# Kernel tuning notes

Hardware: AMD Instinct MI355X
Metric: run time of the kernel (lower is better)

## Reference

```python
import jax, jax.numpy as jnp
import numpy as np

B, N, CIN = 16, 2048, 6
R, G = 20, 128          # Reeb nodes, scc group size
F1 = 1000
NCLASS = 40


def pairwise_distance(pc):
    # pc: (B, N, C) -> adjacency exp(-squared_euclidean_dist), (B, N, N)
    inner = -2.0 * jnp.matmul(pc, pc.transpose(0, 2, 1))
    sq = jnp.sum(pc * pc, axis=-1, keepdims=True)
    return jnp.exp(-(sq + inner + sq.transpose(0, 2, 1)))


def get_laplacian(adj):
    # normalized Laplacian L = I - D^{-1/2} A D^{-1/2}
    d_inv = 1.0 / jnp.sqrt(jnp.sum(adj, axis=-1))
    eye = jnp.eye(adj.shape[-1], dtype=adj.dtype)
    return eye - d_inv[:, :, None] * adj * d_inv[:, None, :]


def cheb_conv(x, L, K, W, b):
    # Chebyshev recurrence: T0=x, T1=Lx, Tk=2L T_{k-1} - T_{k-2}
    xs = [x]
    if K > 1:
        x0, x1 = x, jnp.matmul(L, x)
        xs.append(x1)
        for _ in range(2, K):
            x2 = 2.0 * jnp.matmul(L, x1) - x0
            xs.append(x2)
            x0, x1 = x1, x2
    Bb, Nn, Fin = x.shape
    # torch stacks on dim0 then permutes to (B,N,Fin,K) before reshape -> K is minor axis
    xk = jnp.stack(xs, axis=-1).reshape(Bb, Nn, Fin * K)
    return jnp.matmul(xk, W) + b


def setup_inputs() -> dict:
    key = jax.random.key(0)
    ks = jax.random.split(key, 10)

    def glorot(k, shape):
        lim = np.sqrt(6.0 / (shape[0] + shape[1])).astype(np.float32)
        return jax.random.uniform(k, shape, jnp.float32, -lim, lim)

    return {
        "x": jax.random.normal(ks[0], (B, N, CIN), jnp.float32),
        "laplacian_Reeb": jax.random.normal(ks[1], (B, R, R), jnp.float32),
        "sccs": jax.random.randint(ks[2], (B, R, G), 0, N),
        "W1": glorot(ks[3], (CIN * 3, F1)), "b1": jnp.zeros((F1,), jnp.float32),
        "W2": glorot(ks[4], (F1 * 3, F1)), "b2": jnp.zeros((F1,), jnp.float32),
        "Wr": glorot(ks[5], (F1 * 6, F1)), "br": jnp.zeros((F1,), jnp.float32),
        "Wfc1": glorot(ks[6], (2 * F1, 512)), "bfc1": jnp.zeros((512,), jnp.float32),
        "Wfc2": glorot(ks[7], (512, 128)), "bfc2": jnp.zeros((128,), jnp.float32),
        "Wfc3": glorot(ks[8], (128, NCLASS)), "bfc3": jnp.zeros((NCLASS,), jnp.float32),
        "k": 30, "batch_size": B, "num_points": N,
    }


def reference(x, laplacian_Reeb, sccs, W1, b1, W2, b2, Wr, br,
              Wfc1, bfc1, Wfc2, bfc2, Wfc3, bfc3, k, batch_size, num_points):
    regs = []
    # graph Laplacian from point features (torch.no_grad)
    L = jax.lax.stop_gradient(get_laplacian(pairwise_distance(x)))
    out = jax.nn.relu(cheb_conv(x, L, 3, W1, b1))
    regs.append(jnp.linalg.norm(jnp.matmul(jnp.matmul(out.transpose(0, 2, 1), L), x)))

    # Reeb pooling: per Reeb node, max over its scc vertex group (torch.no_grad)
    v = out[jnp.arange(out.shape[0])[:, None, None], sccs]  # (B, R, G, F1)
    vertices_Reeb = jax.lax.stop_gradient(jnp.max(v, axis=2))  # (B, R, F1)

    # second dynamic-graph Laplacian on features (torch.no_grad)
    L2 = jax.lax.stop_gradient(get_laplacian(pairwise_distance(out)))
    out2 = jax.nn.relu(cheb_conv(out, L2, 3, W2, b2))
    regs.append(jnp.linalg.norm(jnp.matmul(jnp.matmul(out2.transpose(0, 2, 1), L2), x)))

    out_Reeb = jax.nn.relu(cheb_conv(vertices_Reeb, laplacian_Reeb, 6, Wr, br))

    g = jnp.max(out2, axis=1)           # (B, F1) global max pool
    g_Reeb = jnp.max(out_Reeb, axis=1)  # (B, F1)
    feat = jnp.concatenate([g_Reeb, g], axis=1)  # (B, 2000)

    h = jax.nn.relu(jnp.matmul(feat, Wfc1) + bfc1)
    regs += [jnp.sum(Wfc1[:, 0] ** 2), bfc1[0] ** 2]  # norm(weight.data[0])**2
    h = jax.nn.relu(jnp.matmul(h, Wfc2) + bfc2)
    regs += [jnp.sum(Wfc2[:, 0] ** 2), bfc2[0] ** 2]
    out_final = jnp.matmul(h, Wfc3) + bfc3
    regs += [jnp.sum(Wfc3[:, 0] ** 2), bfc3[0] ** 2]

    return out_final, jnp.stack(regs)
```

## Files before the change

### kernel.cpp

```cpp
#include <hip/hip_runtime.h>
#include <stdint.h>

#define DI __device__ __forceinline__

typedef __bf16 bf16x8 __attribute__((ext_vector_type(8)));
typedef float f32x4 __attribute__((ext_vector_type(4)));
typedef unsigned short u16x4 __attribute__((ext_vector_type(4)));
typedef unsigned short u16x8 __attribute__((ext_vector_type(8)));

static constexpr int BB = 16;
static constexpr int NP = 2048;
static constexpr int FP = 1024;
static constexpr int K3 = 3072;
static constexpr int RR = 20;
static constexpr int GG = 128;
static constexpr int RK = 6144;
static constexpr int MRp = 384;
static constexpr int NJ = 32;
static constexpr int NI = 8;
static constexpr int NJ2 = 8;
static constexpr int TPAD = 132;

DI float b2f(unsigned short u) {
    unsigned v = ((unsigned)u) << 16;
    return __builtin_bit_cast(float, v);
}
DI unsigned short f2b(float f) {
    unsigned u = __builtin_bit_cast(unsigned, f);
    unsigned r = (u + 0x7FFFu + ((u >> 16) & 1u)) >> 16;
    return (unsigned short)r;
}

DI void glds16(const unsigned short* g, unsigned short* l) {
    __builtin_amdgcn_global_load_lds(
        (const __attribute__((address_space(1))) void*)g,
        (__attribute__((address_space(3))) void*)l, 16, 0, 0);
}

#define SYNC_VM4() asm volatile("s_waitcnt vmcnt(4)\n\ts_barrier" ::: "memory")
#define SYNC_VM0() asm volatile("s_waitcnt vmcnt(0)\n\ts_barrier" ::: "memory")
#define SYNC_LGKM() asm volatile("s_waitcnt lgkmcnt(0)\n\ts_barrier" ::: "memory")

enum { EADJ = 0, ELAP1 = 1, ELAP2 = 2, EBRELU = 3, EACCR = 4 };

template <int EPI>
__global__ __launch_bounds__(256) void gemm_bt(
    const unsigned short* __restrict__ A, long sA, int lda,
    const unsigned short* __restrict__ Bt, long sB, int ldb,
    unsigned short* __restrict__ C, long sC, int ldc, int K,
    const float* __restrict__ sq,
    float* __restrict__ rowsum,
    const unsigned short* __restrict__ aux, long sAux, int ldaux,
    const float* __restrict__ bias, int biasN)
{
    __shared__ unsigned short smem[128 * TPAD];
    const int tid = threadIdx.x;

    int gx = gridDim.x, gy = gridDim.y;
    int flat = blockIdx.x + gx * (blockIdx.y + gy * blockIdx.z);
    int tpb = gx * gy;
    int T = tpb * gridDim.z;
    int bz, ty, tx;
    if (((T & 7) == 0) && ((gx & 7) == 0)) {
        int per = T >> 3;
        int g = (flat & 7) * per + (flat >> 3);
        bz = g / tpb;
        int t = g - bz * tpb;
        int strip = gy << 3;
        int cg = t / strip;
        int r = t - cg * strip;
        ty = r >> 3;
        tx = (cg << 3) + (r & 7);
    } else {
        bz = blockIdx.z; ty = blockIdx.y; tx = blockIdx.x;
    }
    bool diag = true;
    if (EPI == EADJ) {
        int t = tx;
        int qx = 0;
        while ((qx + 1) * (qx + 2) / 2 <= t) qx++;
        ty = t - qx * (qx + 1) / 2;
        tx = qx;
        diag = (ty == tx);
    }
    const int rowBase = ty * 128;
    const int colBase = tx * 128;
    const unsigned short* Ab;
    const unsigned short* Bb;
    if (EPI == EACCR) {
        Ab = A + (long)rowBase * lda + (long)bz * K;
        Bb = Bt + (long)colBase * ldb + (long)bz * K;
    } else {
        Ab = A + (long)bz * sA + (long)rowBase * lda;
        Bb = Bt + (long)bz * sB + (long)colBase * ldb;
    }

    const int lane = tid & 63;
    const int q = lane >> 4;
    const int l15 = lane & 15;
    const int wave = tid >> 6;
    const int wr = (wave >> 1) * 64;
    const int wc = (wave & 1) * 64;

    const int r0 = tid & 127, c0 = tid >> 7;
    const int c1 = c0 + 2;

    f32x4 acc[4][4];
#pragma unroll
    for (int i = 0; i < 4; i++)
#pragma unroll
        for (int j = 0; j < 4; j++) acc[i][j] = f32x4{0.f, 0.f, 0.f, 0.f};

    const int nIter = K >> 5;
    glds16(Ab + (long)r0 * lda + c0 * 8, smem + tid * 8);
    glds16(Ab + (long)r0 * lda + c1 * 8, smem + (tid + 256) * 8);
    glds16(Bb + (long)r0 * ldb + c0 * 8, smem + 4096 + tid * 8);
    glds16(Bb + (long)r0 * ldb + c1 * 8, smem + 4096 + (tid + 256) * 8);

    for (int it = 0; it < nIter; ++it) {
        unsigned short* cur = smem + ((it & 1) << 13);
        unsigned short* nxt = smem + (((it + 1) & 1) << 13);
        if (it + 1 < nIter) {
            const int kb = (it + 1) << 5;
            glds16(Ab + (long)r0 * lda + kb + c0 * 8, nxt + tid * 8);
            glds16(Ab + (long)r0 * lda + kb + c1 * 8, nxt + (tid + 256) * 8);
            glds16(Bb + (long)r0 * ldb + kb + c0 * 8, nxt + 4096 + tid * 8);
            glds16(Bb + (long)r0 * ldb + kb + c1 * 8, nxt + 4096 + (tid + 256) * 8);
            SYNC_VM4();
        } else {
            SYNC_VM0();
        }
        bf16x8 af[4], bfr[4];
#pragma unroll
        for (int mi = 0; mi < 4; mi++)
            af[mi] = *(const bf16x8*)(cur + (q * 128 + wr + mi * 16 + l15) * 8);
#pragma unroll
        for (int ni = 0; ni < 4; ni++)
            bfr[ni] = *(const bf16x8*)(cur + 4096 + (q * 128 + wc + ni * 16 + l15) * 8);
#pragma unroll
        for (int mi = 0; mi < 4; mi++)
#pragma unroll
            for (int ni = 0; ni < 4; ni++)
                acc[mi][ni] = __builtin_amdgcn_mfma_f32_16x16x32_bf16(
                    af[mi], bfr[ni], acc[mi][ni], 0, 0, 0);
        SYNC_LGKM();
    }

    if (EPI == EADJ) __syncthreads();

    const float* sqb = (EPI == EADJ || EPI == ELAP1 || EPI == ELAP2)
                           ? (sq + (long)bz * NP) : nullptr;
#pragma unroll
    for (int mi = 0; mi < 4; mi++) {
#pragma unroll
        for (int rg = 0; rg < 4; rg++) {
            const int grow = rowBase + wr + mi * 16 + q * 4 + rg;
            float rsumv = 0.f;
            float di = 0.f;
            if (EPI == ELAP1 || EPI == ELAP2) di = sqb[grow];
#pragma unroll
            for (int ni = 0; ni < 4; ni++) {
                const int gcol = colBase + wc + ni * 16 + l15;
                float v = acc[mi][ni][rg];
                long cidx = (long)bz * sC + (long)grow * ldc + gcol;
                if (EPI == EADJ) {
                    float e = __expf(2.f * v - sqb[grow] - sqb[gcol]);
                    unsigned short h = f2b(e);
                    C[cidx] = h;
                    rsumv += e;
                    if (!diag) {
                        const int rl = wr + mi * 16 + q * 4 + rg;
                        const int cl = wc + ni * 16 + l15;
                        smem[cl * TPAD + rl] = h;
                    }
                } else if (EPI == ELAP1) {
                    float o = b2f(aux[(long)bz * sAux + (long)grow * ldaux + gcol]);
                    C[cidx] = f2b(o - di * v);
                } else if (EPI == ELAP2) {
                    long abase = (long)bz * sAux + (long)grow * ldaux + gcol;
                    float o0 = b2f(aux[abase]);
                    float o1 = b2f(aux[abase + 1024]);
                    C[cidx] = f2b(2.f * (o1 - di * v) - o0);
                } else if (EPI == EBRELU) {
                    float bv = (gcol < biasN) ? bias[gcol] : 0.f;
                    float o = v + bv;
                    C[cidx] = f2b(o > 0.f ? o : 0.f);
                } else {
                    atomicAdd(&rowsum[(long)grow * ldc + gcol], v);
                }
            }
            if (EPI == EADJ) {
                rsumv += __shfl_xor(rsumv, 1);
                rsumv += __shfl_xor(rsumv, 2);
                rsumv += __shfl_xor(rsumv, 4);
                rsumv += __shfl_xor(rsumv, 8);
                if (l15 == 0) atomicAdd(&rowsum[(long)bz * NP + grow], rsumv);
            }
        }
    }

    if (EPI == EADJ) {
        if (!diag) {
            __syncthreads();
            const int cl = tid >> 1, hh = tid & 1;
            const unsigned short* srcp = smem + cl * TPAD + hh * 64;
            unsigned short* dstp = C + (long)bz * sC + (long)(colBase + cl) * ldc
                                 + rowBase + hh * 64;
            float csum = 0.f;
#pragma unroll
            for (int k2 = 0; k2 < 8; k2++) {
                u16x4 v0 = *(const u16x4*)(srcp + k2 * 8);
                u16x4 v1 = *(const u16x4*)(srcp + k2 * 8 + 4);
                u16x8 vv;
                vv[0] = v0[0]; vv[1] = v0[1]; vv[2] = v0[2]; vv[3] = v0[3];
                vv[4] = v1[0]; vv[5] = v1[1]; vv[6] = v1[2]; vv[7] = v1[3];
#pragma unroll
                for (int e2 = 0; e2 < 8; e2++) csum += b2f(vv[e2]);
                *(u16x8*)(dstp + k2 * 8) = vv;
            }
            atomicAdd(&rowsum[(long)bz * NP + colBase + cl], csum);
        }
    }
}

__global__ __launch_bounds__(256) void k_trs(
    const unsigned short* __restrict__ src, long sS, int ldS,
    const float* __restrict__ dv,
    unsigned short* __restrict__ dst, long sD, int ldD)
{
    __shared__ unsigned short t[64][72];
    const int b = blockIdx.z;
    const int c0 = blockIdx.x * 64, r0 = blockIdx.y * 64;
    const unsigned short* S = src + (long)b * sS;
    const float* dvb = dv + (long)b * NP;
    unsigned short* D = dst + (long)b * sD;
    const int tx = threadIdx.x & 7, ty = threadIdx.x >> 3;
#pragma unroll
    for (int p = 0; p < 2; p++) {
        int r = ty + p * 32;
        float s = dvb[r0 + r];
        u16x8 v = *(const u16x8*)(S + (long)(r0 + r) * ldS + c0 + tx * 8);
#pragma unroll
        for (int k = 0; k < 8; k++) t[tx * 8 + k][r] = f2b(s * b2f(v[k]));
    }
    __syncthreads();
#pragma unroll
    for (int p = 0; p < 2; p++) {
        int r = ty + p * 32;
        u16x8 v;
#pragma unroll
        for (int k = 0; k < 8; k++) v[k] = t[r][tx * 8 + k];
        *(u16x8*)(D + (long)(c0 + r) * ldD + r0 + tx * 8) = v;
    }
}

__global__ void k_trf32(const float* __restrict__ src, int R, int C,
                        float* __restrict__ dst)
{
    __shared__ float t[32][33];
    const int c0 = blockIdx.x * 32, r0 = blockIdx.y * 32;
#pragma unroll
    for (int p = 0; p < 4; p++) {
        int r = r0 + threadIdx.y + p * 8;
        int c = c0 + threadIdx.x;
        t[threadIdx.y + p * 8][threadIdx.x] =
            (r < R && c < C) ? src[(long)r * C + c] : 0.f;
    }
    __syncthreads();
#pragma unroll
    for (int p = 0; p < 4; p++) {
        int c = c0 + threadIdx.y + p * 8;
        int r = r0 + threadIdx.x;
        if (c < C && r < R) dst[(long)c * R + r] = t[threadIdx.x][threadIdx.y + p * 8];
    }
}

__global__ __launch_bounds__(256) void k_wperm(
    const float* __restrict__ W, unsigned short* __restrict__ dst, int KK, int dstld)
{
    __shared__ float tile[64][65];
    const int o0 = blockIdx.x * 64;
    const int kk0 = blockIdx.y * 64;
    const int s = kk0 >> 10;
    const int fbase = kk0 & 1023;
    const int ci = threadIdx.x & 63;
    const int ri = threadIdx.x >> 6;
#pragma unroll 4
    for (int p = 0; p < 16; p++) {
        int fi = fbase + ri + p * 4;
        int oi = o0 + ci;
        float v = 0.f;
        if (fi < 1000 && oi < 1000) v = W[((long)fi * KK + s) * 1000 + oi];
        tile[ri + p * 4][ci] = v;
    }
    __syncthreads();
#pragma unroll 4
    for (int p = 0; p < 16; p++) {
        int orow = ri + p * 4;
        dst[(long)(o0 + orow) * dstld + kk0 + ci] = f2b(tile[ci][orow]);
    }
}

__global__ void k_zinit(float* __restrict__ rs2, float* __restrict__ g,
                        float* __restrict__ racc, unsigned short* __restrict__ catrpad,
                        float* __restrict__ dv1, float* __restrict__ xacc1,
                        float* __restrict__ xacc2, float* __restrict__ yacc1,
                        float* __restrict__ yacc2, float* __restrict__ l2acc,
                        float* __restrict__ vr, float* __restrict__ sqc,
                        float* __restrict__ accR)
{
    long i = (long)blockIdx.x * 256 + threadIdx.x;
    if (i < (long)BB * NP) { rs2[i] = 0.f; dv1[i] = 0.f; sqc[i] = 0.f; }
    if (i < (long)BB * FP) g[i] = 0.f;
    if (i < 64) racc[i] = 0.f;
    if (i < (long)(MRp - 320) * RK) catrpad[i] = 0;
    if (i < (long)BB * 6 * NP) { xacc1[i] = 0.f; xacc2[i] = 0.f; l2acc[i] = 0.f; }
    if (i < (long)BB * 6 * FP) { yacc1[i] = 0.f; yacc2[i] = 0.f; }
    if (i < (long)BB * RR * FP) vr[i] = 0.f;
    if (i < (long)MRp * FP) accR[i] = 0.f;
}

__global__ void k_xprep(const float* __restrict__ x, float* __restrict__ x6t,
                        float* __restrict__ sqx)
{
    const int b = blockIdx.y;
    const int j = blockIdx.x * 256 + threadIdx.x;
    float s = 0.f;
#pragma unroll
    for (int c = 0; c < 6; c++) {
        float v = x[((long)b * NP + j) * 6 + c];
        x6t[(long)b * 6 * NP + c * NP + j] = v;
        s += v * v;
    }
    sqx[(long)b * NP + j] = s;
}

template <int MODE>
__global__ __launch_bounds__(256) void k_lapj(
    const float* __restrict__ x6t, const float* __restrict__ sqx,
    const float* __restrict__ dv1, const float* __restrict__ srct,
    float* __restrict__ acc)
{
    const int b = blockIdx.z;
    const int row = blockIdx.x * 256 + threadIdx.x;
    const int j0 = blockIdx.y * (NP / NJ);
    const float* xt = x6t + (long)b * 6 * NP;
    const float* sq = sqx + (long)b * NP;
    float xi[6];
#pragma unroll
    for (int c = 0; c < 6; c++) xi[c] = xt[c * NP + row];
    const float sqi = sq[row];
    const float* dv = (MODE >= 1) ? (dv1 + (long)b * NP) : nullptr;
    const float* st = (MODE >= 1) ? (srct + (long)b * 6 * NP) : nullptr;
    float s0 = 0.f;
    float sc[6] = {0, 0, 0, 0, 0, 0};
    for (int j = j0; j < j0 + NP / NJ; j++) {
        float dot = 0.f;
#pragma unroll
        for (int c = 0; c < 6; c++) dot += xi[c] * xt[c * NP + j];
        float e = __expf(2.f * dot - sqi - sq[j]);
        if (MODE == 0) {
            s0 += e;
        } else {
            float wgt = e * dv[j];
#pragma unroll
            for (int c = 0; c < 6; c++) sc[c] += wgt * st[c * NP + j];
        }
    }
    if (MODE == 0) {
        atomicAdd(&acc[(long)b * NP + row], s0);
    } else {
#pragma unroll
        for (int c = 0; c < 6; c++)
            atomicAdd(&acc[(long)b * 6 * NP + c * NP + row], sc[c]);
    }
}

template <int MODE>
__global__ void k_lfin(const float* __restrict__ x6t, const float* __restrict__ dv1,
                       const float* __restrict__ xacc, const float* __restrict__ x1t6,
                       float* __restrict__ outv)
{
    const int b = blockIdx.y;
    const int row = blockIdx.x * 256 + threadIdx.x;
    const float di = dv1[(long)b * NP + row];
#pragma unroll
    for (int c = 0; c < 6; c++) {
        long idx = (long)b * 6 * NP + c * NP + row;
        float xi = x6t[idx];
        float sc = xacc[idx];
        if (MODE == 1) outv[idx] = xi - di * sc;
        else           outv[idx] = 2.f * (x1t6[idx] - di * sc) - xi;
    }
}

__global__ __launch_bounds__(256) void k_adjx(
    const unsigned short* __restrict__ adj, const float* __restrict__ dv,
    const float* __restrict__ x6t, float* __restrict__ l2acc)
{
    __shared__ float xs[6][256];
    __shared__ float dvs[256];
    __shared__ float lsum[64][4][6];
    const int b = blockIdx.z;
    const int j0 = blockIdx.y * (NP / NJ2);
    if (threadIdx.x < 256) dvs[threadIdx.x] = dv[(long)b * NP + j0 + threadIdx.x];
    for (int e = threadIdx.x; e < 6 * 256; e += 256) {
        int c = e >> 8, j = e & 255;
        xs[c][j] = x6t[(long)b * 6 * NP + c * NP + j0 + j];
    }
    __syncthreads();
    const int ty = threadIdx.x >> 2;
    const int tx = threadIdx.x & 3;
    const int grow = blockIdx.x * 64 + ty;
    const unsigned short* rowp = adj + (long)b * NP * NP + (long)grow * NP + j0;
    float sc[6] = {0, 0, 0, 0, 0, 0};
    for (int it = 0; it < 8; it++) {
        int col = it * 32 + tx * 8;
        u16x8 a8 = *(const u16x8*)(rowp + col);
#pragma unroll
        for (int k = 0; k < 8; k++) {
            float w = b2f(a8[k]) * dvs[col + k];
#pragma unroll
            for (int c = 0; c < 6; c++) sc[c] += w * xs[c][col + k];
        }
    }
#pragma unroll
    for (int c = 0; c < 6; c++) lsum[ty][tx][c] = sc[c];
    __syncthreads();
    for (int e = threadIdx.x; e < 64 * 6; e += 256) {
        int row = e / 6, c = e % 6;
        float t = lsum[row][0][c] + lsum[row][1][c] + lsum[row][2][c] + lsum[row][3][c];
        atomicAdd(&l2acc[(long)b * 6 * NP + (long)c * NP + blockIdx.x * 64 + row], t);
    }
}

__global__ __launch_bounds__(256) void k_cheb1(
    const float* __restrict__ x, const float* __restrict__ x1t6,
    const float* __restrict__ x2t6, const float* __restrict__ W1,
    const float* __restrict__ b1, unsigned short* __restrict__ cat,
    float* __restrict__ sqc)
{
    __shared__ float xk[128 * 18];
    __shared__ float rs[128];
    const int b = blockIdx.z;
    const int n0 = blockIdx.x * 128;
    const int f0 = blockIdx.y * 256;
    for (int e = threadIdx.x; e < 128 * 18; e += 256) {
        int rown = e / 18, c18 = e % 18;
        int cc = c18 / 3, kk = c18 % 3;
        int n = n0 + rown;
        float v;
        if (kk == 0) v = x[((long)b * NP + n) * 6 + cc];
        else if (kk == 1) v = x1t6[(long)b * 6 * NP + cc * NP + n];
        else v = x2t6[(long)b * 6 * NP + cc * NP + n];
        xk[e] = v;
    }
    if (threadIdx.x < 128) rs[threadIdx.x] = 0.f;
    __syncthreads();
    const int lane = threadIdx.x & 63;
    for (int gi = threadIdx.x; gi < 128 * 64; gi += 256) {
        int rown = gi >> 6;
        int f4 = f0 + (gi & 63) * 4;
        float a0 = 0, a1 = 0, a2 = 0, a3 = 0;
        if (f4 < 1000) {
            a0 = b1[f4]; a1 = b1[f4 + 1]; a2 = b1[f4 + 2]; a3 = b1[f4 + 3];
#pragma unroll
            for (int cI = 0; cI < 18; cI++) {
                float xv = xk[rown * 18 + cI];
                f32x4 w = *(const f32x4*)(W1 + cI * 1000 + f4);
                a0 += xv * w[0]; a1 += xv * w[1]; a2 += xv * w[2]; a3 += xv * w[3];
            }
            a0 = a0 > 0 ? a0 : 0; a1 = a1 > 0 ? a1 : 0;
            a2 = a2 > 0 ? a2 : 0; a3 = a3 > 0 ? a3 : 0;
        }
        u16x4 o;
        o[0] = f2b(a0); o[1] = f2b(a1); o[2] = f2b(a2); o[3] = f2b(a3);
        *(u16x4*)(cat + (long)b * NP * K3 + (long)(n0 + rown) * K3 + f4) = o;
        float r0 = b2f(o[0]), r1 = b2f(o[1]), r2 = b2f(o[2]), r3 = b2f(o[3]);
        float s2 = r0 * r0 + r1 * r1 + r2 * r2 + r3 * r3;
#pragma unroll
        for (int d = 1; d < 64; d <<= 1) s2 += __shfl_xor(s2, d);
        if (lane == 0) atomicAdd(&rs[rown], s2);
    }
    __syncthreads();
    if (threadIdx.x < 128)
        atomicAdd(&sqc[(long)b * NP + n0 + threadIdx.x], rs[threadIdx.x]);
}

__global__ void k_rsqrt(float* __restrict__ p) {
    int i = blockIdx.x * 256 + threadIdx.x;
    p[i] = rsqrtf(p[i]);
}

__global__ void k_vr(const unsigned short* __restrict__ cat,
                     const int* __restrict__ sccs, float* __restrict__ vr)
{
    const int b = blockIdx.y, r = blockIdx.x;
    const int g0 = blockIdx.z * (GG / 4);
    const int f4 = threadIdx.x * 4;
    const int* sp = sccs + ((long)b * RR + r) * GG;
    float m0 = 0.f, m1 = 0.f, m2 = 0.f, m3 = 0.f;
    for (int g = g0; g < g0 + GG / 4; g++) {
        int idx = sp[g];
        u16x4 v = *(const u16x4*)(cat + ((long)b * NP + idx) * K3 + f4);
        m0 = fmaxf(m0, b2f(v[0])); m1 = fmaxf(m1, b2f(v[1]));
        m2 = fmaxf(m2, b2f(v[2])); m3 = fmaxf(m3, b2f(v[3]));
    }
    float* op = vr + ((long)b * RR + r) * FP + f4;
    atomicMax((int*)&op[0], __float_as_int(m0));
    atomicMax((int*)&op[1], __float_as_int(m1));
    atomicMax((int*)&op[2], __float_as_int(m2));
    atomicMax((int*)&op[3], __float_as_int(m3));
}

__global__ __launch_bounds__(256) void k_reeb(
    const float* __restrict__ vr, const float* __restrict__ lapR,
    unsigned short* __restrict__ catr)
{
    __shared__ float Lr[RR * RR];
    const int b = blockIdx.y;
    for (int e = threadIdx.x; e < RR * RR; e += 256) Lr[e] = lapR[(long)b * RR * RR + e];
    __syncthreads();
    const int f = blockIdx.x * 256 + threadIdx.x;
    float xa[RR], xb[RR], xc[RR];
#pragma unroll
    for (int r = 0; r < RR; r++) xa[r] = vr[((long)b * RR + r) * FP + f];
#pragma unroll
    for (int r = 0; r < RR; r++) catr[((long)b * RR + r) * RK + f] = f2b(xa[r]);
#pragma unroll
    for (int r = 0; r < RR; r++) {
        float s = 0.f;
#pragma unroll
        for (int qq = 0; qq < RR; qq++) s += Lr[r * RR + qq] * xa[qq];
        xb[r] = s;
    }
#pragma unroll
    for (int r = 0; r < RR; r++) catr[((long)b * RR + r) * RK + FP + f] = f2b(xb[r]);
    for (int st = 2; st < 6; st++) {
#pragma unroll
        for (int r = 0; r < RR; r++) {
            float s = 0.f;
#pragma unroll
            for (int qq = 0; qq < RR; qq++) s += Lr[r * RR + qq] * xb[qq];
            xc[r] = 2.f * s - xa[r];
        }
#pragma unroll
        for (int r = 0; r < RR; r++)
            catr[((long)b * RR + r) * RK + st * FP + f] = f2b(xc[r]);
#pragma unroll
        for (int r = 0; r < RR; r++) { xa[r] = xb[r]; xb[r] = xc[r]; }
    }
}

__global__ void k_rfin(const float* __restrict__ accR, const float* __restrict__ br,
                       unsigned short* __restrict__ outr)
{
    const int f = blockIdx.x * 256 + threadIdx.x;
    const int m = blockIdx.y;
    float bv = (f < 1000) ? br[f] : 0.f;
    float v = accR[(long)m * FP + f] + bv;
    outr[(long)m * FP + f] = f2b(v > 0.f ? v : 0.f);
}

__global__ void k_grmax(const unsigned short* __restrict__ outr, float* __restrict__ gr)
{
    const int b = blockIdx.y;
    const int f = blockIdx.x * 256 + threadIdx.x;
    float m = -1e30f;
    for (int r = 0; r < RR; r++)
        m = fmaxf(m, b2f(outr[((long)b * RR + r) * FP + f]));
    gr[(long)b * FP + f] = (f < 1000) ? m : 0.f;
}

__global__ __launch_bounds__(256) void k_rnacc(
    const unsigned short* __restrict__ mat, long sM, int ldm,
    const float* __restrict__ vt6, float* __restrict__ yacc,
    float* __restrict__ gm)
{
    const int b = blockIdx.z;
    const int f = blockIdx.x * 256 + threadIdx.x;
    const int i0 = blockIdx.y * (NP / NI);
    const unsigned short* mp = mat + (long)b * sM + f;
    const float* vp = vt6 + (long)b * 6 * NP;
    float a[6] = {0, 0, 0, 0, 0, 0};
    float mx = 0.f;
    for (int i = i0; i < i0 + NP / NI; i++) {
        float o = b2f(mp[(long)i * ldm]);
        if (gm) mx = fmaxf(mx, o);
#pragma unroll
        for (int c = 0; c < 6; c++) a[c] += o * vp[c * NP + i];
    }
#pragma unroll
    for (int c = 0; c < 6; c++)
        atomicAdd(&yacc[((long)b * 6 + c) * FP + f], a[c]);
    if (gm) atomicMax((int*)&gm[(long)b * FP + f], __float_as_int(mx));
}

__global__ void k_rnred(const float* __restrict__ yacc1,
                        const float* __restrict__ yacc2, float* __restrict__ racc)
{
    __shared__ float red[256];
    const float* y = (blockIdx.x == 0) ? yacc1 : yacc2;
    const long tot = (long)BB * 6 * FP;
    const long per = tot / 16;
    const long e0 = blockIdx.y * per;
    float s = 0.f;
    for (long e = e0 + threadIdx.x; e < e0 + per; e += 256) {
        float v = y[e];
        s += v * v;
    }
    red[threadIdx.x] = s;
    __syncthreads();
    for (int st = 128; st > 0; st >>= 1) {
        if (threadIdx.x < st) red[threadIdx.x] += red[threadIdx.x + st];
        __syncthreads();
    }
    if (threadIdx.x == 0) atomicAdd(&racc[blockIdx.x], red[0]);
}

__global__ __launch_bounds__(256) void k_fc1w(
    const float* __restrict__ gr, const float* __restrict__ g,
    const float* __restrict__ WT1, const float* __restrict__ bias,
    float* __restrict__ h1)
{
    const int b = blockIdx.y;
    const int lane = threadIdx.x & 63;
    const int o = blockIdx.x * 4 + (threadIdx.x >> 6);
    const float* wt = WT1 + (long)o * 2000;
    const float* grp = gr + (long)b * FP;
    const float* gp = g + (long)b * FP;
    float s = 0.f;
    for (int j0 = 0; j0 < 2000; j0 += 64) {
        int j = j0 + lane;
        if (j < 2000) {
            float fv = (j < 1000) ? grp[j] : gp[j - 1000];
            s += fv * wt[j];
        }
    }
#pragma unroll
    for (int d = 1; d < 64; d <<= 1) s += __shfl_xor(s, d);
    if (lane == 0) {
        float v = s + bias[o];
        h1[(long)b * 512 + o] = v > 0.f ? v : 0.f;
    }
}

__global__ __launch_bounds__(256) void k_fc2w(
    const float* __restrict__ h1, const float* __restrict__ WT2,
    const float* __restrict__ bias, float* __restrict__ h2)
{
    const int b = blockIdx.y;
    const int lane = threadIdx.x & 63;
    const int o = blockIdx.x * 4 + (threadIdx.x >> 6);
    const float* wt = WT2 + (long)o * 512;
    const float* hp = h1 + (long)b * 512;
    float s = 0.f;
#pragma unroll
    for (int j0 = 0; j0 < 512; j0 += 64) s += hp[j0 + lane] * wt[j0 + lane];
#pragma unroll
    for (int d = 1; d < 64; d <<= 1) s += __shfl_xor(s, d);
    if (lane == 0) {
        float v = s + bias[o];
        h2[(long)b * 128 + o] = v > 0.f ? v : 0.f;
    }
}

__global__ void k_tail(const float* __restrict__ h2, const float* __restrict__ Wfc3,
                       const float* __restrict__ bfc3, const float* __restrict__ Wfc1,
                       const float* __restrict__ bfc1, const float* __restrict__ Wfc2,
                       const float* __restrict__ bfc2, const float* __restrict__ racc,
                       float* __restrict__ out)
{
    if (blockIdx.x == 0) {
        for (int e = threadIdx.x; e < 640; e += 256) {
            int row = e / 40, o = e % 40;
            float s = bfc3[o];
            for (int j = 0; j < 128; j++) s += h2[row * 128 + j] * Wfc3[j * 40 + o];
            out[e] = s;
        }
        return;
    }
    __shared__ float red[256];
    float s = 0.f;
    if (blockIdx.x == 1) {
        for (int j = threadIdx.x; j < 2000; j += 256) { float w = Wfc1[j * 512]; s += w * w; }
    } else if (blockIdx.x == 2) {
        for (int j = threadIdx.x; j < 512; j += 256) { float w = Wfc2[j * 128]; s += w * w; }
    } else {
        for (int j = threadIdx.x; j < 128; j += 256) { float w = Wfc3[j * 40]; s += w * w; }
    }
    red[threadIdx.x] = s;
    __syncthreads();
    for (int st = 128; st > 0; st >>= 1) {
        if (threadIdx.x < st) red[threadIdx.x] += red[threadIdx.x + st];
        __syncthreads();
    }
    if (threadIdx.x == 0) {
        if (blockIdx.x == 1) out[642] = red[0];
        else if (blockIdx.x == 2) out[644] = red[0];
        else {
            out[646] = red[0];
            out[640] = sqrtf(racc[0]);
            out[641] = sqrtf(racc[1]);
            out[643] = bfc1[0] * bfc1[0];
            out[645] = bfc2[0] * bfc2[0];
            out[647] = bfc3[0] * bfc3[0];
        }
    }
}

extern "C" void kernel_launch(void* const* d_in, const int* in_sizes, int n_in,
                              void* d_out, int out_size, void* d_ws, size_t ws_size,
                              hipStream_t stream)
{
    (void)in_sizes; (void)n_in; (void)out_size;
    const float* x    = (const float*)d_in[0];
    const float* lapR = (const float*)d_in[1];
    const int*   sccs = (const int*)d_in[2];
    const float* W1   = (const float*)d_in[3];
    const float* b1   = (const float*)d_in[4];
    const float* W2   = (const float*)d_in[5];
    const float* b2   = (const float*)d_in[6];
    const float* Wr   = (const float*)d_in[7];
    const float* br   = (const float*)d_in[8];
    const float* Wfc1 = (const float*)d_in[9];
    const float* bfc1 = (const float*)d_in[10];
    const float* Wfc2 = (const float*)d_in[11];
    const float* bfc2 = (const float*)d_in[12];
    const float* Wfc3 = (const float*)d_in[13];
    const float* bfc3 = (const float*)d_in[14];
    float* out = (float*)d_out;

    char* w = (char*)d_ws;
    size_t used = 0;
    auto alloc = [&](size_t bytes) {
        char* p = w + used;
        used += (bytes + 255) & ~(size_t)255;
        return p;
    };
    unsigned short* w2pt = (unsigned short*)alloc((size_t)FP * K3 * 2);
    unsigned short* wrpt = (unsigned short*)alloc((size_t)FP * RK * 2);
    unsigned short* catr = (unsigned short*)alloc((size_t)MRp * RK * 2);
    unsigned short* outr = (unsigned short*)alloc((size_t)MRp * FP * 2);
    float* accR = (float*)alloc((size_t)MRp * FP * 4);
    float* vr   = (float*)alloc((size_t)BB * RR * FP * 4);
    float* x6t  = (float*)alloc((size_t)BB * 6 * NP * 4);
    float* sqx  = (float*)alloc((size_t)BB * NP * 4);
    float* dv1  = (float*)alloc((size_t)BB * NP * 4);
    float* x1t6 = (float*)alloc((size_t)BB * 6 * NP * 4);
    float* x2t6 = (float*)alloc((size_t)BB * 6 * NP * 4);
    float* xacc1= (float*)alloc((size_t)BB * 6 * NP * 4);
    float* xacc2= (float*)alloc((size_t)BB * 6 * NP * 4);
    float* l2acc= (float*)alloc((size_t)BB * 6 * NP * 4);
    float* sqc  = (float*)alloc((size_t)BB * NP * 4);
    float* rs2  = (float*)alloc((size_t)BB * NP * 4);
    float* l2xt6= (float*)alloc((size_t)BB * 6 * NP * 4);
    float* g    = (float*)alloc((size_t)BB * FP * 4);
    float* gr   = (float*)alloc((size_t)BB * FP * 4);
    float* h1   = (float*)alloc((size_t)BB * 512 * 4);
    float* h2   = (float*)alloc((size_t)BB * 128 * 4);
    float* racc = (float*)alloc(256);
    float* WT1  = (float*)alloc((size_t)512 * 2000 * 4);
    float* WT2  = (float*)alloc((size_t)128 * 512 * 4);
    float* yacc1= (float*)alloc((size_t)BB * 6 * FP * 4);
    float* yacc2= (float*)alloc((size_t)BB * 6 * FP * 4);

    const size_t PCAT = (size_t)NP * K3 * 2;
    const size_t PA   = (size_t)NP * NP * 2;
    const size_t PTT  = (size_t)FP * NP * 2;
    int C = 16;
    while (C > 1 && used + (size_t)C * (PCAT + PA + PTT) + 4096 > ws_size) C >>= 1;
    if (used + (size_t)C * (PCAT + PA + PTT) + 4096 > ws_size) return;

    unsigned short* cat_c = (unsigned short*)alloc((size_t)C * PCAT);
    unsigned short* a_c   = (unsigned short*)alloc((size_t)C * PA);
    unsigned short* tt_c  = (unsigned short*)alloc((size_t)C * PTT);
    unsigned short* out2_c = a_c;

    const long sCat = (long)NP * K3;
    const long sL2  = (long)NP * NP;
    const long sTT  = (long)FP * NP;
    const long sO2  = (long)NP * FP;

    k_zinit<<<dim3(1536), 256, 0, stream>>>(rs2, g, racc, catr + (size_t)320 * RK,
                                            dv1, xacc1, xacc2, yacc1, yacc2, l2acc,
                                            vr, sqc, accR);

    k_wperm<<<dim3(16, K3 / 64), 256, 0, stream>>>(W2, w2pt, 3, K3);
    k_wperm<<<dim3(16, RK / 64), 256, 0, stream>>>(Wr, wrpt, 6, RK);
    k_trf32<<<dim3(16, 63), dim3(32, 8), 0, stream>>>(Wfc1, 2000, 512, WT1);
    k_trf32<<<dim3(4, 16), dim3(32, 8), 0, stream>>>(Wfc2, 512, 128, WT2);

    k_xprep<<<dim3(8, BB), 256, 0, stream>>>(x, x6t, sqx);
    k_lapj<0><<<dim3(8, NJ, BB), 256, 0, stream>>>(x6t, sqx, nullptr, nullptr, dv1);
    k_rsqrt<<<dim3(BB * NP / 256), 256, 0, stream>>>(dv1);
    k_lapj<1><<<dim3(8, NJ, BB), 256, 0, stream>>>(x6t, sqx, dv1, x6t, xacc1);
    k_lfin<1><<<dim3(8, BB), 256, 0, stream>>>(x6t, dv1, xacc1, nullptr, x1t6);
    k_lapj<2><<<dim3(8, NJ, BB), 256, 0, stream>>>(x6t, sqx, dv1, x1t6, xacc2);
    k_lfin<2><<<dim3(8, BB), 256, 0, stream>>>(x6t, dv1, xacc2, x1t6, x2t6);

    for (int c0 = 0; c0 < BB; c0 += C) {
        const float* xc  = x     + (long)c0 * NP * 6;
        const float* x6c = x6t   + (long)c0 * 6 * NP;
        const float* x1c = x1t6  + (long)c0 * 6 * NP;
        const float* x2c = x2t6  + (long)c0 * 6 * NP;
        float*       sqcc= sqc   + (long)c0 * NP;
        float*       rsc = rs2   + (long)c0 * NP;
        float*       l2ac= l2acc + (long)c0 * 6 * NP;
        float*       l2xc= l2xt6 + (long)c0 * 6 * NP;

        k_cheb1<<<dim3(16, 4, C), 256, 0, stream>>>(xc, x1c, x2c, W1, b1, cat_c, sqcc);

        gemm_bt<EADJ><<<dim3(136, 1, C), 256, 0, stream>>>(
            cat_c, sCat, K3, cat_c, sCat, K3, a_c, sL2, NP, FP,
            sqcc, rsc, nullptr, 0, 0, nullptr, 0);
        k_rsqrt<<<dim3(C * NP / 256), 256, 0, stream>>>(rsc);

        k_adjx<<<dim3(NP / 64, NJ2, C), 256, 0, stream>>>(a_c, rsc, x6c, l2ac);
        k_lfin<1><<<dim3(8, C), 256, 0, stream>>>(x6c, rsc, l2ac, nullptr, l2xc);

        k_trs<<<dim3(16, 32, C), 256, 0, stream>>>(cat_c, sCat, K3, rsc, tt_c, sTT, NP);
        gemm_bt<ELAP1><<<dim3(8, 16, C), 256, 0, stream>>>(
            a_c, sL2, NP, tt_c, sTT, NP, cat_c + 1024, sCat, K3, NP,
            rsc, nullptr, cat_c, sCat, K3, nullptr, 0);

        k_trs<<<dim3(16, 32, C), 256, 0, stream>>>(cat_c + 1024, sCat, K3, rsc, tt_c, sTT, NP);
        gemm_bt<ELAP2><<<dim3(8, 16, C), 256, 0, stream>>>(
            a_c, sL2, NP, tt_c, sTT, NP, cat_c + 2048, sCat, K3, NP,
            rsc, nullptr, cat_c, sCat, K3, nullptr, 0);

        gemm_bt<EBRELU><<<dim3(8, 16, C), 256, 0, stream>>>(
            cat_c, sCat, K3, w2pt, 0, K3, out2_c, sO2, FP, K3,
            nullptr, nullptr, nullptr, 0, 0, b2, 1000);

        k_vr<<<dim3(RR, C, 4), 256, 0, stream>>>(
            cat_c, sccs + (long)c0 * RR * GG, vr + (long)c0 * RR * FP);
        k_rnacc<<<dim3(4, NI, C), 256, 0, stream>>>(
            cat_c, sCat, K3, x1c, yacc1 + (long)c0 * 6 * FP, nullptr);
        k_rnacc<<<dim3(4, NI, C), 256, 0, stream>>>(
            out2_c, sO2, FP, l2xc, yacc2 + (long)c0 * 6 * FP, g + (long)c0 * FP);
    }

    k_reeb<<<dim3(4, BB), 256, 0, stream>>>(vr, lapR, catr);
    gemm_bt<EACCR><<<dim3(8, 3, 4), 256, 0, stream>>>(
        catr, 0, RK, wrpt, 0, RK, outr, 0, FP, RK / 4,
        nullptr, accR, nullptr, 0, 0, nullptr, 0);
    k_rfin<<<dim3(4, 320), 256, 0, stream>>>(accR, br, outr);
    k_grmax<<<dim3(4, BB), 256, 0, stream>>>(outr, gr);

    k_rnred<<<dim3(2, 16), 256, 0, stream>>>(yacc1, yacc2, racc);
    k_fc1w<<<dim3(128, BB), 256, 0, stream>>>(gr, g, WT1, bfc1, h1);
    k_fc2w<<<dim3(32, BB), 256, 0, stream>>>(h1, WT2, bfc2, h2);
    k_tail<<<dim3(4), 256, 0, stream>>>(h2, Wfc3, bfc3, Wfc1, bfc1, Wfc2, bfc2, racc, out);
}
```

Before: 1.955 ms.

## Triple-buffer GEMM K-loop and fuse Reeb bias-ReLU with max pooling

The GEMM main loop moves from double to triple buffering in LDS. Each tile is now prefetched two iterations ahead, and one barrier per iteration is dropped: the trailing lgkmcnt wait plus barrier is removed, since a third buffer keeps reuse safe. Separately, the Reeb bias+ReLU pass and the per-batch max pool are fused into one kernel, which removes the outr intermediate buffer and a launch. The shared memory footprint grows to 48KB per block, which may lower occupancy.

```diff
diff --git a/kernel.cpp b/kernel.cpp
--- a/kernel.cpp
+++ b/kernel.cpp
@@ -39,7 +39,6 @@
 
 #define SYNC_VM4() asm volatile("s_waitcnt vmcnt(4)\n\ts_barrier" ::: "memory")
 #define SYNC_VM0() asm volatile("s_waitcnt vmcnt(0)\n\ts_barrier" ::: "memory")
-#define SYNC_LGKM() asm volatile("s_waitcnt lgkmcnt(0)\n\ts_barrier" ::: "memory")
 
 enum { EADJ = 0, ELAP1 = 1, ELAP2 = 2, EBRELU = 3, EACCR = 4 };
 
@@ -53,7 +52,7 @@
     const unsigned short* __restrict__ aux, long sAux, int ldaux,
     const float* __restrict__ bias, int biasN)
 {
-    __shared__ unsigned short smem[128 * TPAD];
+    __shared__ unsigned short smem[24576];
     const int tid = threadIdx.x;
 
     int gx = gridDim.x, gy = gridDim.y;
@@ -112,38 +111,47 @@
         for (int j = 0; j < 4; j++) acc[i][j] = f32x4{0.f, 0.f, 0.f, 0.f};
 
     const int nIter = K >> 5;
-    glds16(Ab + (long)r0 * lda + c0 * 8, smem + tid * 8);
-    glds16(Ab + (long)r0 * lda + c1 * 8, smem + (tid + 256) * 8);
-    glds16(Bb + (long)r0 * ldb + c0 * 8, smem + 4096 + tid * 8);
-    glds16(Bb + (long)r0 * ldb + c1 * 8, smem + 4096 + (tid + 256) * 8);
-
-    for (int it = 0; it < nIter; ++it) {
-        unsigned short* cur = smem + ((it & 1) << 13);
-        unsigned short* nxt = smem + (((it + 1) & 1) << 13);
-        if (it + 1 < nIter) {
-            const int kb = (it + 1) << 5;
-            glds16(Ab + (long)r0 * lda + kb + c0 * 8, nxt + tid * 8);
-            glds16(Ab + (long)r0 * lda + kb + c1 * 8, nxt + (tid + 256) * 8);
-            glds16(Bb + (long)r0 * ldb + kb + c0 * 8, nxt + 4096 + tid * 8);
-            glds16(Bb + (long)r0 * ldb + kb + c1 * 8, nxt + 4096 + (tid + 256) * 8);
+
+    auto stage = [&](int tile, int bsel) {
+        unsigned short* dst = smem + bsel * 8192;
+        const int kb = tile << 5;
+        glds16(Ab + (long)r0 * lda + kb + c0 * 8, dst + tid * 8);
+        glds16(Ab + (long)r0 * lda + kb + c1 * 8, dst + (tid + 256) * 8);
+        glds16(Bb + (long)r0 * ldb + kb + c0 * 8, dst + 4096 + tid * 8);
+        glds16(Bb + (long)r0 * ldb + kb + c1 * 8, dst + 4096 + (tid + 256) * 8);
+    };
+    auto compute = [&](int bsel) {
+        unsigned short* cur = smem + bsel * 8192;
+        bf16x8 af[4], bfr[4];
+#pragma unroll
+        for (int mi = 0; mi < 4; mi++)
+            af[mi] = *(const bf16x8*)(cur + (q * 128 + wr + mi * 16 + l15) * 8);
+#pragma unroll
+        for (int ni = 0; ni < 4; ni++)
+            bfr[ni] = *(const bf16x8*)(cur + 4096 + (q * 128 + wc + ni * 16 + l15) * 8);
+#pragma unroll
+        for (int mi = 0; mi < 4; mi++)
+#pragma unroll
+            for (int ni = 0; ni < 4; ni++)
+                acc[mi][ni] = __builtin_amdgcn_mfma_f32_16x16x32_bf16(
+                    af[mi], bfr[ni], acc[mi][ni], 0, 0, 0);
+    };
+
+    stage(0, 0);
+    stage(1, 1);
+    int cb = 0, sb = 2;
+    for (int t = 0; t < nIter; ++t) {
+        if (t + 2 < nIter) {
+            SYNC_VM4();
+            stage(t + 2, sb);
+        } else if (t + 2 == nIter) {
             SYNC_VM4();
         } else {
             SYNC_VM0();
         }
-        bf16x8 af[4], bfr[4];
-#pragma unroll
-        for (int mi = 0; mi < 4; mi++)
-            af[mi] = *(const bf16x8*)(cur + (q * 128 + wr + mi * 16 + l15) * 8);
-#pragma unroll
-        for (int ni = 0; ni < 4; ni++)
-            bfr[ni] = *(const bf16x8*)(cur + 4096 + (q * 128 + wc + ni * 16 + l15) * 8);
-#pragma unroll
-        for (int mi = 0; mi < 4; mi++)
-#pragma unroll
-            for (int ni = 0; ni < 4; ni++)
-                acc[mi][ni] = __builtin_amdgcn_mfma_f32_16x16x32_bf16(
-                    af[mi], bfr[ni], acc[mi][ni], 0, 0, 0);
-        SYNC_LGKM();
+        compute(cb);
+        cb = (cb == 2) ? 0 : cb + 1;
+        sb = (sb == 2) ? 0 : sb + 1;
     }
 
     if (EPI == EADJ) __syncthreads();
@@ -552,24 +560,20 @@
     }
 }
 
-__global__ void k_rfin(const float* __restrict__ accR, const float* __restrict__ br,
-                       unsigned short* __restrict__ outr)
-{
-    const int f = blockIdx.x * 256 + threadIdx.x;
-    const int m = blockIdx.y;
-    float bv = (f < 1000) ? br[f] : 0.f;
-    float v = accR[(long)m * FP + f] + bv;
-    outr[(long)m * FP + f] = f2b(v > 0.f ? v : 0.f);
-}
-
-__global__ void k_grmax(const unsigned short* __restrict__ outr, float* __restrict__ gr)
+__global__ void k_rgr(const float* __restrict__ accR, const float* __restrict__ br,
+                      float* __restrict__ gr)
 {
     const int b = blockIdx.y;
     const int f = blockIdx.x * 256 + threadIdx.x;
+    if (f >= 1000) { gr[(long)b * FP + f] = 0.f; return; }
+    const float bv = br[f];
     float m = -1e30f;
-    for (int r = 0; r < RR; r++)
-        m = fmaxf(m, b2f(outr[((long)b * RR + r) * FP + f]));
-    gr[(long)b * FP + f] = (f < 1000) ? m : 0.f;
+    for (int r = 0; r < RR; r++) {
+        float v = accR[((long)b * RR + r) * FP + f] + bv;
+        v = v > 0.f ? v : 0.f;
+        m = fmaxf(m, b2f(f2b(v)));
+    }
+    gr[(long)b * FP + f] = m;
 }
 
 __global__ __launch_bounds__(256) void k_rnacc(
@@ -741,7 +745,6 @@
     unsigned short* w2pt = (unsigned short*)alloc((size_t)FP * K3 * 2);
     unsigned short* wrpt = (unsigned short*)alloc((size_t)FP * RK * 2);
     unsigned short* catr = (unsigned short*)alloc((size_t)MRp * RK * 2);
-    unsigned short* outr = (unsigned short*)alloc((size_t)MRp * FP * 2);
     float* accR = (float*)alloc((size_t)MRp * FP * 4);
     float* vr   = (float*)alloc((size_t)BB * RR * FP * 4);
     float* x6t  = (float*)alloc((size_t)BB * 6 * NP * 4);
@@ -843,10 +846,9 @@
 
     k_reeb<<<dim3(4, BB), 256, 0, stream>>>(vr, lapR, catr);
     gemm_bt<EACCR><<<dim3(8, 3, 4), 256, 0, stream>>>(
-        catr, 0, RK, wrpt, 0, RK, outr, 0, FP, RK / 4,
+        catr, 0, RK, wrpt, 0, RK, nullptr, 0, FP, RK / 4,
         nullptr, accR, nullptr, 0, 0, nullptr, 0);
-    k_rfin<<<dim3(4, 320), 256, 0, stream>>>(accR, br, outr);
-    k_grmax<<<dim3(4, BB), 256, 0, stream>>>(outr, gr);
+    k_rgr<<<dim3(4, BB), 256, 0, stream>>>(accR, br, gr);
 
     k_rnred<<<dim3(2, 16), 256, 0, stream>>>(yacc1, yacc2, racc);
     k_fc1w<<<dim3(128, BB), 256, 0, stream>>>(gr, g, WT1, bfc1, h1);
```

After: 1.957 ms. About the same (+0.1%).

## Add 256x128-tile GEMM for Laplacian and W2 products; fuse Reeb bias-relu-max

Applied to the files above, without the earlier changes.

Adds a gemm_bt2 kernel with 256x128 output tiles, four waves each computing 64x128, and double-buffered async global-to-LDS staging. The ELAP1, ELAP2 and EBRELU GEMMs move to this kernel on half as many blocks, so each loaded A and B fragment feeds more MFMAs. Separately, the Reeb bias+ReLU pass and the per-batch max are merged into one kernel, which drops the outr buffer and one launch. The larger tiles cost more registers and LDS per block and reduce the number of blocks in flight.

```diff
diff --git a/kernel.cpp b/kernel.cpp
--- a/kernel.cpp
+++ b/kernel.cpp
@@ -38,6 +38,7 @@
 }
 
 #define SYNC_VM4() asm volatile("s_waitcnt vmcnt(4)\n\ts_barrier" ::: "memory")
+#define SYNC_VM6() asm volatile("s_waitcnt vmcnt(6)\n\ts_barrier" ::: "memory")
 #define SYNC_VM0() asm volatile("s_waitcnt vmcnt(0)\n\ts_barrier" ::: "memory")
 #define SYNC_LGKM() asm volatile("s_waitcnt lgkmcnt(0)\n\ts_barrier" ::: "memory")
 
@@ -48,12 +49,11 @@
     const unsigned short* __restrict__ A, long sA, int lda,
     const unsigned short* __restrict__ Bt, long sB, int ldb,
     unsigned short* __restrict__ C, long sC, int ldc, int K,
-    const float* __restrict__ sq,
-    float* __restrict__ rowsum,
+    const float* __restrict__ sq, float* __restrict__ rowsum,
     const unsigned short* __restrict__ aux, long sAux, int ldaux,
     const float* __restrict__ bias, int biasN)
 {
-    __shared__ unsigned short smem[128 * TPAD];
+    __shared__ unsigned short smem[17024];
     const int tid = threadIdx.x;
 
     int gx = gridDim.x, gy = gridDim.y;
@@ -148,22 +148,19 @@
 
     if (EPI == EADJ) __syncthreads();
 
-    const float* sqb = (EPI == EADJ || EPI == ELAP1 || EPI == ELAP2)
-                           ? (sq + (long)bz * NP) : nullptr;
+    const float* sqb = (EPI == EADJ) ? (sq + (long)bz * NP) : nullptr;
 #pragma unroll
     for (int mi = 0; mi < 4; mi++) {
 #pragma unroll
         for (int rg = 0; rg < 4; rg++) {
             const int grow = rowBase + wr + mi * 16 + q * 4 + rg;
             float rsumv = 0.f;
-            float di = 0.f;
-            if (EPI == ELAP1 || EPI == ELAP2) di = sqb[grow];
 #pragma unroll
             for (int ni = 0; ni < 4; ni++) {
                 const int gcol = colBase + wc + ni * 16 + l15;
                 float v = acc[mi][ni][rg];
-                long cidx = (long)bz * sC + (long)grow * ldc + gcol;
                 if (EPI == EADJ) {
+                    long cidx = (long)bz * sC + (long)grow * ldc + gcol;
                     float e = __expf(2.f * v - sqb[grow] - sqb[gcol]);
                     unsigned short h = f2b(e);
                     C[cidx] = h;
@@ -173,18 +170,6 @@
                         const int cl = wc + ni * 16 + l15;
                         smem[cl * TPAD + rl] = h;
                     }
-                } else if (EPI == ELAP1) {
-                    float o = b2f(aux[(long)bz * sAux + (long)grow * ldaux + gcol]);
-                    C[cidx] = f2b(o - di * v);
-                } else if (EPI == ELAP2) {
-                    long abase = (long)bz * sAux + (long)grow * ldaux + gcol;
-                    float o0 = b2f(aux[abase]);
-                    float o1 = b2f(aux[abase + 1024]);
-                    C[cidx] = f2b(2.f * (o1 - di * v) - o0);
-                } else if (EPI == EBRELU) {
-                    float bv = (gcol < biasN) ? bias[gcol] : 0.f;
-                    float o = v + bv;
-                    C[cidx] = f2b(o > 0.f ? o : 0.f);
                 } else {
                     atomicAdd(&rowsum[(long)grow * ldc + gcol], v);
                 }
@@ -199,26 +184,147 @@
         }
     }
 
-    if (EPI == EADJ) {
-        if (!diag) {
-            __syncthreads();
-            const int cl = tid >> 1, hh = tid & 1;
-            const unsigned short* srcp = smem + cl * TPAD + hh * 64;
-            unsigned short* dstp = C + (long)bz * sC + (long)(colBase + cl) * ldc
-                                 + rowBase + hh * 64;
-            float csum = 0.f;
-#pragma unroll
-            for (int k2 = 0; k2 < 8; k2++) {
-                u16x4 v0 = *(const u16x4*)(srcp + k2 * 8);
-                u16x4 v1 = *(const u16x4*)(srcp + k2 * 8 + 4);
-                u16x8 vv;
-                vv[0] = v0[0]; vv[1] = v0[1]; vv[2] = v0[2]; vv[3] = v0[3];
-                vv[4] = v1[0]; vv[5] = v1[1]; vv[6] = v1[2]; vv[7] = v1[3];
-#pragma unroll
-                for (int e2 = 0; e2 < 8; e2++) csum += b2f(vv[e2]);
-                *(u16x8*)(dstp + k2 * 8) = vv;
+    if (EPI == EADJ && !diag) {
+        __syncthreads();
+        const int cl = tid >> 1, hh = tid & 1;
+        const unsigned short* srcp = smem + cl * TPAD + hh * 64;
+        unsigned short* dstp = C + (long)bz * sC + (long)(colBase + cl) * ldc
+                             + rowBase + hh * 64;
+        float csum = 0.f;
+#pragma unroll
+        for (int k2 = 0; k2 < 8; k2++) {
+            u16x4 v0 = *(const u16x4*)(srcp + k2 * 8);
+            u16x4 v1 = *(const u16x4*)(srcp + k2 * 8 + 4);
+            u16x8 vv;
+            vv[0] = v0[0]; vv[1] = v0[1]; vv[2] = v0[2]; vv[3] = v0[3];
+            vv[4] = v1[0]; vv[5] = v1[1]; vv[6] = v1[2]; vv[7] = v1[3];
+#pragma unroll
+            for (int e2 = 0; e2 < 8; e2++) csum += b2f(vv[e2]);
+            *(u16x8*)(dstp + k2 * 8) = vv;
+        }
+        atomicAdd(&rowsum[(long)bz * NP + colBase + cl], csum);
+    }
+}
+
+template <int EPI>
+__global__ __launch_bounds__(256) void gemm_bt2(
+    const unsigned short* __restrict__ A, long sA, int lda,
+    const unsigned short* __restrict__ Bt, long sB, int ldb,
+    unsigned short* __restrict__ C, long sC, int ldc, int K,
+    const float* __restrict__ dv,
+    const unsigned short* __restrict__ aux, long sAux, int ldaux,
+    const float* __restrict__ bias, int biasN)
+{
+    __shared__ unsigned short smem[24576];
+    const int tid = threadIdx.x;
+
+    int gx = gridDim.x, gy = gridDim.y;
+    int flat = blockIdx.x + gx * (blockIdx.y + gy * blockIdx.z);
+    int tpb = gx * gy;
+    int T = tpb * gridDim.z;
+    int bz, ty, tx;
+    if (((T & 7) == 0) && ((gx & 7) == 0)) {
+        int per = T >> 3;
+        int g = (flat & 7) * per + (flat >> 3);
+        bz = g / tpb;
+        int t = g - bz * tpb;
+        int strip = gy << 3;
+        int cg = t / strip;
+        int r = t - cg * strip;
+        ty = r >> 3;
+        tx = (cg << 3) + (r & 7);
+    } else {
+        bz = blockIdx.z; ty = blockIdx.y; tx = blockIdx.x;
+    }
+    const int rowBase = ty * 256;
+    const int colBase = tx * 128;
+    const unsigned short* Ab = A + (long)bz * sA + (long)rowBase * lda;
+    const unsigned short* Bb = Bt + (long)bz * sB + (long)colBase * ldb;
+
+    const int lane = tid & 63;
+    const int q = lane >> 4;
+    const int l15 = lane & 15;
+    const int wave = tid >> 6;
+    const int brow = tid & 127;
+    const int bch = tid >> 7;
+
+    f32x4 acc[4][8];
+#pragma unroll
+    for (int i = 0; i < 4; i++)
+#pragma unroll
+        for (int j = 0; j < 8; j++) acc[i][j] = f32x4{0.f, 0.f, 0.f, 0.f};
+
+    const int nIter = K >> 5;
+
+    auto stage = [&](int tile, unsigned short* dst) {
+        const int kb = tile << 5;
+#pragma unroll
+        for (int ci = 0; ci < 4; ci++)
+            glds16(Ab + (long)tid * lda + kb + ci * 8, dst + (ci * 256 + tid) * 8);
+#pragma unroll
+        for (int j = 0; j < 2; j++) {
+            int ch = bch + j * 2;
+            glds16(Bb + (long)brow * ldb + kb + ch * 8,
+                   dst + 8192 + (ch * 128 + brow) * 8);
+        }
+    };
+    auto compute = [&](unsigned short* cur) {
+        bf16x8 af[4], bfr[8];
+#pragma unroll
+        for (int mi = 0; mi < 4; mi++)
+            af[mi] = *(const bf16x8*)(cur + (q * 256 + wave * 64 + mi * 16 + l15) * 8);
+#pragma unroll
+        for (int ni = 0; ni < 8; ni++)
+            bfr[ni] = *(const bf16x8*)(cur + 8192 + (q * 128 + ni * 16 + l15) * 8);
+#pragma unroll
+        for (int mi = 0; mi < 4; mi++)
+#pragma unroll
+            for (int ni = 0; ni < 8; ni++)
+                acc[mi][ni] = __builtin_amdgcn_mfma_f32_16x16x32_bf16(
+                    af[mi], bfr[ni], acc[mi][ni], 0, 0, 0);
+    };
+
+    stage(0, smem);
+    for (int it = 0; it < nIter; ++it) {
+        unsigned short* cur = smem + ((it & 1) ? 12288 : 0);
+        unsigned short* nxt = smem + ((it & 1) ? 0 : 12288);
+        if (it + 1 < nIter) {
+            stage(it + 1, nxt);
+            SYNC_VM6();
+        } else {
+            SYNC_VM0();
+        }
+        compute(cur);
+        SYNC_LGKM();
+    }
+
+    const float* dvb = (EPI != EBRELU) ? (dv + (long)bz * NP) : nullptr;
+#pragma unroll
+    for (int mi = 0; mi < 4; mi++) {
+#pragma unroll
+        for (int rg = 0; rg < 4; rg++) {
+            const int grow = rowBase + wave * 64 + mi * 16 + q * 4 + rg;
+            float di = 0.f;
+            if (EPI == ELAP1 || EPI == ELAP2) di = dvb[grow];
+#pragma unroll
+            for (int ni = 0; ni < 8; ni++) {
+                const int gcol = colBase + ni * 16 + l15;
+                float v = acc[mi][ni][rg];
+                long cidx = (long)bz * sC + (long)grow * ldc + gcol;
+                if (EPI == ELAP1) {
+                    float o = b2f(aux[(long)bz * sAux + (long)grow * ldaux + gcol]);
+                    C[cidx] = f2b(o - di * v);
+                } else if (EPI == ELAP2) {
+                    long abase = (long)bz * sAux + (long)grow * ldaux + gcol;
+                    float o0 = b2f(aux[abase]);
+                    float o1 = b2f(aux[abase + 1024]);
+                    C[cidx] = f2b(2.f * (o1 - di * v) - o0);
+                } else {
+                    float bv = (gcol < biasN) ? bias[gcol] : 0.f;
+                    float o = v + bv;
+                    C[cidx] = f2b(o > 0.f ? o : 0.f);
+                }
             }
-            atomicAdd(&rowsum[(long)bz * NP + colBase + cl], csum);
         }
     }
 }
@@ -552,24 +658,20 @@
     }
 }
 
-__global__ void k_rfin(const float* __restrict__ accR, const float* __restrict__ br,
-                       unsigned short* __restrict__ outr)
-{
-    const int f = blockIdx.x * 256 + threadIdx.x;
-    const int m = blockIdx.y;
-    float bv = (f < 1000) ? br[f] : 0.f;
-    float v = accR[(long)m * FP + f] + bv;
-    outr[(long)m * FP + f] = f2b(v > 0.f ? v : 0.f);
-}
-
-__global__ void k_grmax(const unsigned short* __restrict__ outr, float* __restrict__ gr)
+__global__ void k_rgr(const float* __restrict__ accR, const float* __restrict__ br,
+                      float* __restrict__ gr)
 {
     const int b = blockIdx.y;
     const int f = blockIdx.x * 256 + threadIdx.x;
+    if (f >= 1000) { gr[(long)b * FP + f] = 0.f; return; }
+    const float bv = br[f];
     float m = -1e30f;
-    for (int r = 0; r < RR; r++)
-        m = fmaxf(m, b2f(outr[((long)b * RR + r) * FP + f]));
-    gr[(long)b * FP + f] = (f < 1000) ? m : 0.f;
+    for (int r = 0; r < RR; r++) {
+        float v = accR[((long)b * RR + r) * FP + f] + bv;
+        v = v > 0.f ? v : 0.f;
+        m = fmaxf(m, b2f(f2b(v)));
+    }
+    gr[(long)b * FP + f] = m;
 }
 
 __global__ __launch_bounds__(256) void k_rnacc(
@@ -741,7 +843,6 @@
     unsigned short* w2pt = (unsigned short*)alloc((size_t)FP * K3 * 2);
     unsigned short* wrpt = (unsigned short*)alloc((size_t)FP * RK * 2);
     unsigned short* catr = (unsigned short*)alloc((size_t)MRp * RK * 2);
-    unsigned short* outr = (unsigned short*)alloc((size_t)MRp * FP * 2);
     float* accR = (float*)alloc((size_t)MRp * FP * 4);
     float* vr   = (float*)alloc((size_t)BB * RR * FP * 4);
     float* x6t  = (float*)alloc((size_t)BB * 6 * NP * 4);
@@ -820,18 +921,18 @@
         k_lfin<1><<<dim3(8, C), 256, 0, stream>>>(x6c, rsc, l2ac, nullptr, l2xc);
 
         k_trs<<<dim3(16, 32, C), 256, 0, stream>>>(cat_c, sCat, K3, rsc, tt_c, sTT, NP);
-        gemm_bt<ELAP1><<<dim3(8, 16, C), 256, 0, stream>>>(
+        gemm_bt2<ELAP1><<<dim3(8, 8, C), 256, 0, stream>>>(
             a_c, sL2, NP, tt_c, sTT, NP, cat_c + 1024, sCat, K3, NP,
-            rsc, nullptr, cat_c, sCat, K3, nullptr, 0);
+            rsc, cat_c, sCat, K3, nullptr, 0);
 
         k_trs<<<dim3(16, 32, C), 256, 0, stream>>>(cat_c + 1024, sCat, K3, rsc, tt_c, sTT, NP);
-        gemm_bt<ELAP2><<<dim3(8, 16, C), 256, 0, stream>>>(
+        gemm_bt2<ELAP2><<<dim3(8, 8, C), 256, 0, stream>>>(
             a_c, sL2, NP, tt_c, sTT, NP, cat_c + 2048, sCat, K3, NP,
-            rsc, nullptr, cat_c, sCat, K3, nullptr, 0);
-
-        gemm_bt<EBRELU><<<dim3(8, 16, C), 256, 0, stream>>>(
+            rsc, cat_c, sCat, K3, nullptr, 0);
+
+        gemm_bt2<EBRELU><<<dim3(8, 8, C), 256, 0, stream>>>(
             cat_c, sCat, K3, w2pt, 0, K3, out2_c, sO2, FP, K3,
-            nullptr, nullptr, nullptr, 0, 0, b2, 1000);
+            nullptr, nullptr, 0, 0, b2, 1000);
 
         k_vr<<<dim3(RR, C, 4), 256, 0, stream>>>(
             cat_c, sccs + (long)c0 * RR * GG, vr + (long)c0 * RR * FP);
@@ -843,10 +944,9 @@
 
     k_reeb<<<dim3(4, BB), 256, 0, stream>>>(vr, lapR, catr);
     gemm_bt<EACCR><<<dim3(8, 3, 4), 256, 0, stream>>>(
-        catr, 0, RK, wrpt, 0, RK, outr, 0, FP, RK / 4,
+        catr, 0, RK, wrpt, 0, RK, nullptr, 0, FP, RK / 4,
         nullptr, accR, nullptr, 0, 0, nullptr, 0);
-    k_rfin<<<dim3(4, 320), 256, 0, stream>>>(accR, br, outr);
-    k_grmax<<<dim3(4, BB), 256, 0, stream>>>(outr, gr);
+    k_rgr<<<dim3(4, BB), 256, 0, stream>>>(accR, br, gr);
 
     k_rnred<<<dim3(2, 16), 256, 0, stream>>>(yacc1, yacc2, racc);
     k_fc1w<<<dim3(128, BB), 256, 0, stream>>>(gr, g, WT1, bfc1, h1);
```

After: 1.960 ms. Within noise of the previous version (+0.2%).
